# Optimization experiments

Hardware: AMD Instinct MI355X
Metric: run time of the kernel (lower is better)

## Reference

```python
import jax, jax.numpy as jnp
import numpy as np

B, T, D = 32, 512, 384
DUR_MAX = 8                 # durations drawn in [0, DUR_MAX)
MAX_OUT = T * (DUR_MAX - 1) # static upper bound on total expanded length (3584)
ALPHA = 1.0


def setup_inputs() -> dict:
    key = jax.random.key(0)
    k1, k2 = jax.random.split(key)
    x = jax.random.normal(k1, (B, T, D), dtype=jnp.float32)
    durations = jax.random.randint(k2, (B, T), 0, DUR_MAX, dtype=jnp.int32)
    return {"input": x, "durations": durations}


def reference(input, durations):
    # patched_dur = clamp(round(alpha * dur), min=0)
    patched = jnp.round(ALPHA * durations.astype(jnp.float32)).astype(jnp.int32)
    patched = jnp.maximum(patched, 0)                       # [B, T]
    cum = jnp.cumsum(patched, axis=1)                       # [B, T] exclusive-right boundaries
    total = cum[:, -1:]                                      # [B, 1] true expanded lengths

    pos = jnp.arange(MAX_OUT, dtype=jnp.int32)               # [MAX_OUT]
    # output frame j comes from token idx = first t with cum[t] > j
    idx = jax.vmap(lambda c: jnp.searchsorted(c, pos, side='right'))(cum)  # [B, MAX_OUT]
    idx = jnp.clip(idx, 0, T - 1)
    valid = pos[None, :] < total                              # [B, MAX_OUT]

    out = jnp.take_along_axis(input, idx[:, :, None], axis=1)  # [B, MAX_OUT, D]
    return jnp.where(valid[:, :, None], out, jnp.zeros((), dtype=input.dtype))
```

## Files before the change

### kernel.cpp

```cpp
#include <hip/hip_runtime.h>

#define NB 32
#define NT 512
#define ND 384
#define DUR_MAX 8
#define MAX_OUT (NT * (DUR_MAX - 1))
#define NV (ND / 4)

__global__ __launch_bounds__(NT) void lr_scan_scatter(
    const int* __restrict__ dur, int* __restrict__ totals, int* __restrict__ idxmap)
{
    __shared__ int s[NT];
    const int b = blockIdx.x;
    const int t = threadIdx.x;

    int d = dur[b * NT + t];
    d = d > 0 ? d : 0;
    s[t] = d;
    __syncthreads();

    #pragma unroll
    for (int off = 1; off < NT; off <<= 1) {
        int v = (t >= off) ? s[t - off] : 0;
        __syncthreads();
        s[t] += v;
        __syncthreads();
    }
    const int cum = s[t];
    const int start = cum - d;

    int* base = idxmap + b * MAX_OUT;
    for (int j = 0; j < d; ++j) base[start + j] = t;

    if (t == NT - 1) totals[b] = cum;
}

__global__ __launch_bounds__(256) void lr_gather(
    const float4* __restrict__ in, const int* __restrict__ totals,
    const int* __restrict__ idxmap, float4* __restrict__ out)
{
    const unsigned g = blockIdx.x * 256u + threadIdx.x;
    const unsigned row = g / NV;
    const unsigned col = g - row * NV;
    const unsigned b = row / MAX_OUT;
    const unsigned pos = row - b * MAX_OUT;

    float4 r = make_float4(0.f, 0.f, 0.f, 0.f);
    if ((int)pos < totals[b]) {
        const int idx = idxmap[row];
        r = in[(b * NT + idx) * NV + col];
    }
    out[g] = r;
}

extern "C" void kernel_launch(void* const* d_in, const int* in_sizes, int n_in,
                              void* d_out, int out_size, void* d_ws, size_t ws_size,
                              hipStream_t stream)
{
    const float* x   = (const float*)d_in[0];
    const int*   dur = (const int*)d_in[1];
    float* out = (float*)d_out;

    int* totals = (int*)d_ws;
    int* idxmap = (int*)((char*)d_ws + 128);

    lr_scan_scatter<<<NB, NT, 0, stream>>>(dur, totals, idxmap);

    const unsigned n_vec = (unsigned)NB * MAX_OUT * NV;
    lr_gather<<<n_vec / 256, 256, 0, stream>>>(
        (const float4*)x, totals, idxmap, (float4*)out);
}
```

Before: 203.8 us.

## Use wave-shuffle scan, encode padding in idxmap, swizzle gather workgroups

The scan kernel now uses intra-wavefront shuffle prefix sums plus a small shared per-wave total instead of a 9-step shared-memory scan with barriers. The index map stores precomputed float4 source offsets and writes -1 for padding frames, so the gather no longer loads a per-batch total or recomputes the batch and position. Gather workgroup IDs are also remapped across 8 groups, apparently to spread consecutive blocks over XCDs. The scatter kernel now writes the whole map, and the swizzle may reduce locality in the read stream.

```diff
diff --git a/kernel.cpp b/kernel.cpp
--- a/kernel.cpp
+++ b/kernel.cpp
@@ -6,50 +6,58 @@
 #define DUR_MAX 8
 #define MAX_OUT (NT * (DUR_MAX - 1))
 #define NV (ND / 4)
+#define NWG ((NB * MAX_OUT * NV) / 256)
 
 __global__ __launch_bounds__(NT) void lr_scan_scatter(
-    const int* __restrict__ dur, int* __restrict__ totals, int* __restrict__ idxmap)
+    const int* __restrict__ dur, int* __restrict__ idxmap)
 {
-    __shared__ int s[NT];
-    const int b = blockIdx.x;
-    const int t = threadIdx.x;
+    __shared__ int wsum[NT / 64];
+    const int b    = blockIdx.x;
+    const int t    = threadIdx.x;
+    const int lane = t & 63;
+    const int w    = t >> 6;
 
     int d = dur[b * NT + t];
     d = d > 0 ? d : 0;
-    s[t] = d;
+
+    int v = d;
+    #pragma unroll
+    for (int off = 1; off < 64; off <<= 1) {
+        int u = __shfl_up(v, off);
+        if (lane >= off) v += u;
+    }
+    if (lane == 63) wsum[w] = v;
     __syncthreads();
-
-    #pragma unroll
-    for (int off = 1; off < NT; off <<= 1) {
-        int v = (t >= off) ? s[t - off] : 0;
-        __syncthreads();
-        s[t] += v;
-        __syncthreads();
+    if (t == 0) {
+        int acc = 0;
+        #pragma unroll
+        for (int i = 0; i < NT / 64; ++i) { acc += wsum[i]; wsum[i] = acc; }
     }
-    const int cum = s[t];
+    __syncthreads();
+    const int cum   = v + (w ? wsum[w - 1] : 0);
+    const int total = wsum[NT / 64 - 1];
     const int start = cum - d;
 
     int* base = idxmap + b * MAX_OUT;
-    for (int j = 0; j < d; ++j) base[start + j] = t;
-
-    if (t == NT - 1) totals[b] = cum;
+    const int src = (b * NT + t) * NV;
+    for (int j = 0; j < d; ++j) base[start + j] = src;
+    for (int s = total + t; s < MAX_OUT; s += NT) base[s] = -1;
 }
 
 __global__ __launch_bounds__(256) void lr_gather(
-    const float4* __restrict__ in, const int* __restrict__ totals,
-    const int* __restrict__ idxmap, float4* __restrict__ out)
+    const float4* __restrict__ in, const int* __restrict__ idxmap,
+    float4* __restrict__ out)
 {
-    const unsigned g = blockIdx.x * 256u + threadIdx.x;
+    const unsigned bid = blockIdx.x;
+    const unsigned per = NWG / 8;
+    const unsigned swz = (bid & 7u) * per + (bid >> 3);
+    const unsigned g   = swz * 256u + threadIdx.x;
     const unsigned row = g / NV;
     const unsigned col = g - row * NV;
-    const unsigned b = row / MAX_OUT;
-    const unsigned pos = row - b * MAX_OUT;
 
+    const int src = idxmap[row];
     float4 r = make_float4(0.f, 0.f, 0.f, 0.f);
-    if ((int)pos < totals[b]) {
-        const int idx = idxmap[row];
-        r = in[(b * NT + idx) * NV + col];
-    }
+    if (src >= 0) r = in[src + col];
     out[g] = r;
 }
 
@@ -61,12 +69,8 @@
     const int*   dur = (const int*)d_in[1];
     float* out = (float*)d_out;
 
-    int* totals = (int*)d_ws;
-    int* idxmap = (int*)((char*)d_ws + 128);
+    int* idxmap = (int*)d_ws;
 
-    lr_scan_scatter<<<NB, NT, 0, stream>>>(dur, totals, idxmap);
-
-    const unsigned n_vec = (unsigned)NB * MAX_OUT * NV;
-    lr_gather<<<n_vec / 256, 256, 0, stream>>>(
-        (const float4*)x, totals, idxmap, (float4*)out);
+    lr_scan_scatter<<<NB, NT, 0, stream>>>(dur, idxmap);
+    lr_gather<<<NWG, 256, 0, stream>>>((const float4*)x, idxmap, (float4*)out);
 }
```

Measured after the change: 197.9 us. 2.9% less time.
